# Optimization experiments

Measured on AMD Instinct MI355X. Metric: run time of the kernel, lower is better.

The kernel has to match this reference:

```python
import jax, jax.numpy as jnp
import numpy as np

E = 64          # num_routed_experts
K = 6           # num_experts_per_token
NS = 2          # num_shared_experts
D = 512         # hidden_size
F = 512         # expert_intermediate_size = intermediate_size // 4


def setup_inputs() -> dict:
    key = jax.random.key(0)
    ks = jax.random.split(key, 8)
    s = 0.02
    return {
        "hidden_states": jax.random.normal(ks[0], (2, 1024, D), dtype=jnp.float32),
        "Wr": jax.random.normal(ks[1], (D, E), dtype=jnp.float32) * s,      # router
        "sWg": jax.random.normal(ks[2], (NS, D, F), dtype=jnp.float32) * s,  # shared gate_proj
        "sWu": jax.random.normal(ks[3], (NS, D, F), dtype=jnp.float32) * s,  # shared up_proj
        "sWd": jax.random.normal(ks[4], (NS, F, D), dtype=jnp.float32) * s,  # shared down_proj
        "Wg": jax.random.normal(ks[5], (E, D, F), dtype=jnp.float32) * s,    # routed gate_proj
        "Wu": jax.random.normal(ks[6], (E, D, F), dtype=jnp.float32) * s,    # routed up_proj
        "Wd": jax.random.normal(ks[7], (E, F, D), dtype=jnp.float32) * s,    # routed down_proj
    }


def _swiglu_ffn(x, wg, wu, wd):
    # x: (N, D); wg/wu: (D, F); wd: (F, D)
    return (jax.nn.silu(x @ wg) * (x @ wu)) @ wd


def reference(hidden_states, Wr, sWg, sWu, sWd, Wg, Wu, Wd):
    B, S, d = hidden_states.shape
    x = hidden_states.reshape(-1, d)  # (N, D)
    N = x.shape[0]

    # ---- shared experts (always on) ----
    shared = jnp.zeros_like(x)
    for e in range(NS):
        shared = shared + _swiglu_ffn(x, sWg[e], sWu[e], sWd[e])

    # ---- top-k router ----
    logits = x @ Wr                                   # (N, E)
    probs = jax.nn.softmax(logits, axis=-1)
    top_w, top_i = jax.lax.top_k(probs, K)            # (N, K)
    top_w = top_w / jnp.sum(top_w, axis=-1, keepdims=True)  # renormalize
    gate = jnp.zeros((N, E), dtype=x.dtype).at[jnp.arange(N)[:, None], top_i].set(top_w)

    # ---- routed experts: per-expert FFN, combined with sparse gate ----
    routed = jnp.zeros_like(x)
    for e in range(E):
        routed = routed + _swiglu_ffn(x, Wg[e], Wu[e], Wd[e]) * gate[:, e:e + 1]

    out = (shared + routed + x).reshape(B, S, d)
    return out
```

## Files before the change

kernel.cpp:

```cpp
#include <hip/hip_runtime.h>

#define N_TOK 2048
#define DD 512
#define FF 512
#define EE 64
#define TK 6
#define NG 66
#define RSLOT 12288
#define NSLOT 16384
#define BM 64
#define BN 64
#define BK 64
#define NKT 8
#define MAXT 320
#define MATSZ 262144

typedef float f32x4 __attribute__((ext_vector_type(4)));
typedef __bf16 bf16x8 __attribute__((ext_vector_type(8)));

__device__ __forceinline__ unsigned cvtpk(float lo, float hi) {
  unsigned r;
  asm("v_cvt_pk_bf16_f32 %0, %1, %2" : "=v"(r) : "v"(lo), "v"(hi));
  return r;
}

__device__ __forceinline__ void gll16(const void* g, void* l) {
  __builtin_amdgcn_global_load_lds(
      (const __attribute__((address_space(1))) unsigned int*)g,
      (__attribute__((address_space(3))) unsigned int*)l, 16, 0, 0);
}

__global__ __launch_bounds__(256) void convw_k(
    const float* __restrict__ Wg, const float* __restrict__ Wu, const float* __restrict__ Wd,
    const float* __restrict__ sWg, const float* __restrict__ sWu, const float* __restrict__ sWd,
    short* __restrict__ Wt) {
  int y = blockIdx.y;
  int kind = y / 66, idx = y % 66;
  const float* src;
  if (kind == 0)      src = (idx < EE) ? Wg + (size_t)idx * MATSZ : sWg + (size_t)(idx - EE) * MATSZ;
  else if (kind == 1) src = (idx < EE) ? Wu + (size_t)idx * MATSZ : sWu + (size_t)(idx - EE) * MATSZ;
  else                src = (idx < EE) ? Wd + (size_t)idx * MATSZ : sWd + (size_t)(idx - EE) * MATSZ;
  short* dst = Wt + (size_t)y * MATSZ;
  int f0 = blockIdx.x * 64;
  int lane = threadIdx.x & 63, w = threadIdx.x >> 6;
  int fl = lane & 15, dg = lane >> 4;
  const float* sp = src + (size_t)(dg * 8) * 512 + f0 + fl * 4;
  short* dp = dst + (size_t)(f0 + fl * 4) * 512 + dg * 8;
#pragma unroll 1
  for (int it = 0; it < 4; ++it) {
    int db = (it * 4 + w) * 32;
    f32x4 v[8];
#pragma unroll
    for (int jd = 0; jd < 8; ++jd)
      v[jd] = *(const f32x4*)(sp + (size_t)(db + jd) * 512);
#pragma unroll
    for (int jf = 0; jf < 4; ++jf) {
      uint4 o;
      o.x = cvtpk(v[0][jf], v[1][jf]);
      o.y = cvtpk(v[2][jf], v[3][jf]);
      o.z = cvtpk(v[4][jf], v[5][jf]);
      o.w = cvtpk(v[6][jf], v[7][jf]);
      *(uint4*)(dp + (size_t)jf * 512 + db) = o;
    }
  }
}

__global__ void convx_k(const float* __restrict__ x, short* __restrict__ Xb) {
  int i = blockIdx.x * 256 + threadIdx.x;
  const f32x4* p = (const f32x4*)(x + (size_t)i * 8);
  f32x4 v0 = p[0], v1 = p[1];
  uint4 o;
  o.x = cvtpk(v0[0], v0[1]); o.y = cvtpk(v0[2], v0[3]);
  o.z = cvtpk(v1[0], v1[1]); o.w = cvtpk(v1[2], v1[3]);
  *(uint4*)&Xb[(size_t)i * 8] = o;
}

__global__ __launch_bounds__(256) void router_k(
    const float* __restrict__ x, const float* __restrict__ Wr,
    int* __restrict__ top_i, float* __restrict__ top_w, int* __restrict__ cnt) {
  __shared__ float xs[16 * 512];
  __shared__ float part[4][16][64];
  int tid = threadIdx.x, lane = tid & 63, w = tid >> 6;
  int t0 = blockIdx.x * 16;
  const f32x4* xin = (const f32x4*)(x + (size_t)t0 * DD);
  f32x4* xs4 = (f32x4*)xs;
#pragma unroll
  for (int i = 0; i < 8; ++i) xs4[i * 256 + tid] = xin[i * 256 + tid];
  __syncthreads();
  float acc[16];
#pragma unroll
  for (int t = 0; t < 16; ++t) acc[t] = 0.f;
  for (int kk = 0; kk < 32; ++kk) {
    int k = w * 128 + kk * 4;
    float w0 = Wr[(size_t)(k + 0) * EE + lane];
    float w1 = Wr[(size_t)(k + 1) * EE + lane];
    float w2 = Wr[(size_t)(k + 2) * EE + lane];
    float w3 = Wr[(size_t)(k + 3) * EE + lane];
#pragma unroll
    for (int t = 0; t < 16; ++t) {
      f32x4 xv = *(const f32x4*)&xs[t * 512 + k];
      acc[t] = fmaf(xv[0], w0, acc[t]);
      acc[t] = fmaf(xv[1], w1, acc[t]);
      acc[t] = fmaf(xv[2], w2, acc[t]);
      acc[t] = fmaf(xv[3], w3, acc[t]);
    }
  }
#pragma unroll
  for (int t = 0; t < 16; ++t) part[w][t][lane] = acc[t];
  __syncthreads();
#pragma unroll
  for (int tt = 0; tt < 4; ++tt) {
    int t = w * 4 + tt;
    float l0 = part[0][t][lane] + part[1][t][lane] + part[2][t][lane] + part[3][t][lane];
    float m = l0;
#pragma unroll
    for (int s = 32; s; s >>= 1) m = fmaxf(m, __shfl_xor(m, s));
    float p = __expf(l0 - m);
    int wi[TK]; float wv[TK];
#pragma unroll
    for (int it = 0; it < TK; ++it) {
      float v = p;
#pragma unroll
      for (int s = 32; s; s >>= 1) v = fmaxf(v, __shfl_xor(v, s));
      unsigned long long b = __ballot(p == v);
      int idx = __ffsll((unsigned long long)b) - 1;
      wi[it] = idx; wv[it] = v;
      if (lane == idx) p = -1.f;
    }
    float wsum = 0.f;
#pragma unroll
    for (int it = 0; it < TK; ++it) wsum += wv[it];
    int tg = t0 + t;
    if (lane < TK) {
      int si = 0; float sv = 0.f;
#pragma unroll
      for (int it = 0; it < TK; ++it) if (lane == it) { si = wi[it]; sv = wv[it]; }
      top_i[tg * TK + lane] = si;
      top_w[tg * TK + lane] = sv / wsum;
      atomicAdd(&cnt[si], 1);
    }
  }
}

__global__ void offsets_k(const int* __restrict__ cnt, int* __restrict__ goff,
                          int* __restrict__ fill, int* __restrict__ wk_g,
                          int* __restrict__ wk_mt, int* __restrict__ nitems) {
  int i = threadIdx.x;
  fill[i] = 0;
  int c = cnt[i];
  int s = c;
#pragma unroll
  for (int d = 1; d < 64; d <<= 1) { int t = __shfl_up(s, d); if (i >= d) s += t; }
  goff[i] = s - c;
  if (i == 63) {
    goff[EE] = RSLOT;
    goff[EE + 1] = RSLOT + N_TOK;
    goff[EE + 2] = RSLOT + 2 * N_TOK;
  }
  int nt = (c + BM - 1) >> 6;
  int ts = nt;
#pragma unroll
  for (int d = 1; d < 64; d <<= 1) { int t = __shfl_up(ts, d); if (i >= d) ts += t; }
  int texcl = ts - nt;
  for (int t = 0; t < nt; ++t) { wk_g[texcl + t] = i; wk_mt[texcl + t] = t; }
  int tot = __shfl(ts, 63);
  wk_g[tot + i] = EE + (i >> 5);
  wk_mt[tot + i] = i & 31;
  if (i == 0) nitems[0] = tot + 64;
}

__global__ void scatter_k(const int* __restrict__ top_i, const float* __restrict__ top_w,
                          const int* __restrict__ goff, int* __restrict__ fill,
                          int* __restrict__ btok, float* __restrict__ bw) {
  int idx = blockIdx.x * blockDim.x + threadIdx.x;
  if (idx < RSLOT) {
    int e = top_i[idx];
    int pos = goff[e] + atomicAdd(&fill[e], 1);
    btok[pos] = idx / TK;
    bw[pos] = top_w[idx];
  } else if (idx < NSLOT) {
    int j = idx - RSLOT;
    btok[idx] = j & (N_TOK - 1);
    bw[idx] = 1.0f;
  }
}

__global__ void initout_k(const float* __restrict__ x, float* __restrict__ out, int n4) {
  int i = blockIdx.x * blockDim.x + threadIdx.x;
  if (i < n4) reinterpret_cast<f32x4*>(out)[i] = reinterpret_cast<const f32x4*>(x)[i];
}

__global__ __launch_bounds__(256) void gemm1_k(
    const short* __restrict__ Xb, const short* __restrict__ Wtg, const short* __restrict__ Wtu,
    const int* __restrict__ goff, const int* __restrict__ btok,
    const int* __restrict__ wk_g, const int* __restrict__ wk_mt,
    const int* __restrict__ nitems, short* __restrict__ H) {
  int item = blockIdx.y;
  if (item >= nitems[0]) return;
  int g = wk_g[item], mt = wk_mt[item];
  int s0g = goff[g], cnt = goff[g + 1] - s0g;
  int n0 = blockIdx.x * BN;
  const short* gmat = Wtg + (size_t)g * MATSZ;
  const short* umat = Wtu + (size_t)g * MATSZ;

  __shared__ __align__(16) short lds[2][12288];

  int tid = threadIdx.x, lane = tid & 63, w = tid >> 6;
  int wr = w >> 1, wc = w & 1;
  int lr = lane & 15, lgq = lane >> 4;
  int s0 = s0g + mt * BM;

  const short* sp[6];
  int ldst[6];
#pragma unroll
  for (int q = 0; q < 6; ++q) {
    int c = w * 6 + q;
    ldst[q] = c * 512;
    int rl = (c & 7) * 8 + (lane >> 3);
    int u = (lane & 7) ^ (rl & 7);
    if (c < 8) {
      int slot = (mt * BM + rl < cnt) ? s0 + rl : s0;
      sp[q] = Xb + (size_t)btok[slot] * 512 + u * 8;
    } else if (c < 16) {
      sp[q] = gmat + (size_t)(n0 + rl) * 512 + u * 8;
    } else {
      sp[q] = umat + (size_t)(n0 + rl) * 512 + u * 8;
    }
  }

  f32x4 accg[2][2], accu[2][2];
#pragma unroll
  for (int i = 0; i < 2; ++i)
#pragma unroll
    for (int j = 0; j < 2; ++j) {
      accg[i][j] = f32x4{0.f, 0.f, 0.f, 0.f};
      accu[i][j] = f32x4{0.f, 0.f, 0.f, 0.f};
    }

  auto STAGE = [&](int b, int kt) {
#pragma unroll
    for (int q = 0; q < 6; ++q) gll16(sp[q] + kt * 64, &lds[b][ldst[q]]);
  };
  auto COMPUTE = [&](int b) {
    const short* L = lds[b];
#pragma unroll
    for (int ks = 0; ks < 2; ++ks) {
      bf16x8 af[2], bg[2], bu[2];
#pragma unroll
      for (int i = 0; i < 2; ++i) {
        int row = wr * 32 + i * 16 + lr;
        af[i] = *(const bf16x8*)&L[row * 64 + (((ks * 4 + lgq) ^ (row & 7)) * 8)];
      }
#pragma unroll
      for (int j = 0; j < 2; ++j) {
        int fr = wc * 32 + j * 16 + lr;
        int o = fr * 64 + (((ks * 4 + lgq) ^ (fr & 7)) * 8);
        bg[j] = *(const bf16x8*)&L[4096 + o];
        bu[j] = *(const bf16x8*)&L[8192 + o];
      }
#pragma unroll
      for (int i = 0; i < 2; ++i)
#pragma unroll
        for (int j = 0; j < 2; ++j) {
          accg[i][j] = __builtin_amdgcn_mfma_f32_16x16x32_bf16(af[i], bg[j], accg[i][j], 0, 0, 0);
          accu[i][j] = __builtin_amdgcn_mfma_f32_16x16x32_bf16(af[i], bu[j], accu[i][j], 0, 0, 0);
        }
    }
  };

  STAGE(0, 0);
  __syncthreads();
  int b = 0;
#pragma unroll 1
  for (int kt = 0; kt < NKT; ++kt) {
    if (kt + 1 < NKT) STAGE(b ^ 1, kt + 1);
    COMPUTE(b);
    __syncthreads();
    b ^= 1;
  }

#pragma unroll
  for (int i = 0; i < 2; ++i)
#pragma unroll
    for (int j = 0; j < 2; ++j)
#pragma unroll
      for (int r = 0; r < 4; ++r) {
        int mrow = wr * 32 + i * 16 + lgq * 4 + r;
        if (mt * BM + mrow < cnt) {
          float gg = accg[i][j][r];
          float uu = accu[i][j][r];
          float hv = (gg / (1.f + __expf(-gg))) * uu;
          int col = n0 + wc * 32 + j * 16 + lr;
          H[(size_t)(s0 + mrow) * FF + col] = (short)(cvtpk(hv, hv) & 0xffffu);
        }
      }
}

__global__ __launch_bounds__(256) void gemm2_k(
    const short* __restrict__ H, const short* __restrict__ Wtd,
    const int* __restrict__ goff, const int* __restrict__ btok, const float* __restrict__ bw,
    const int* __restrict__ wk_g, const int* __restrict__ wk_mt,
    const int* __restrict__ nitems, float* __restrict__ out) {
  int item = blockIdx.y;
  if (item >= nitems[0]) return;
  int g = wk_g[item], mt = wk_mt[item];
  int s0g = goff[g], cnt = goff[g + 1] - s0g;
  int n0 = blockIdx.x * BN;
  const short* dmat = Wtd + (size_t)g * MATSZ;

  __shared__ __align__(16) short lds[2][8192];

  int tid = threadIdx.x, lane = tid & 63, w = tid >> 6;
  int wr = w >> 1, wc = w & 1;
  int lr = lane & 15, lgq = lane >> 4;
  int s0 = s0g + mt * BM;

  const short* sp[4];
  int ldst[4];
#pragma unroll
  for (int q = 0; q < 4; ++q) {
    int c = w * 4 + q;
    ldst[q] = c * 512;
    int rl = (c & 7) * 8 + (lane >> 3);
    int u = (lane & 7) ^ (rl & 7);
    if (c < 8) {
      int slot = (mt * BM + rl < cnt) ? s0 + rl : s0;
      sp[q] = H + (size_t)slot * 512 + u * 8;
    } else {
      sp[q] = dmat + (size_t)(n0 + rl) * 512 + u * 8;
    }
  }

  f32x4 acc[2][2];
#pragma unroll
  for (int i = 0; i < 2; ++i)
#pragma unroll
    for (int j = 0; j < 2; ++j) acc[i][j] = f32x4{0.f, 0.f, 0.f, 0.f};

  auto STAGE = [&](int b, int kt) {
#pragma unroll
    for (int q = 0; q < 4; ++q) gll16(sp[q] + kt * 64, &lds[b][ldst[q]]);
  };
  auto COMPUTE = [&](int b) {
    const short* L = lds[b];
#pragma unroll
    for (int ks = 0; ks < 2; ++ks) {
      bf16x8 af[2], bd[2];
#pragma unroll
      for (int i = 0; i < 2; ++i) {
        int row = wr * 32 + i * 16 + lr;
        af[i] = *(const bf16x8*)&L[row * 64 + (((ks * 4 + lgq) ^ (row & 7)) * 8)];
      }
#pragma unroll
      for (int j = 0; j < 2; ++j) {
        int dr = wc * 32 + j * 16 + lr;
        bd[j] = *(const bf16x8*)&L[4096 + dr * 64 + (((ks * 4 + lgq) ^ (dr & 7)) * 8)];
      }
#pragma unroll
      for (int i = 0; i < 2; ++i)
#pragma unroll
        for (int j = 0; j < 2; ++j)
          acc[i][j] = __builtin_amdgcn_mfma_f32_16x16x32_bf16(af[i], bd[j], acc[i][j], 0, 0, 0);
    }
  };

  STAGE(0, 0);
  __syncthreads();
  int b = 0;
#pragma unroll 1
  for (int kt = 0; kt < NKT; ++kt) {
    if (kt + 1 < NKT) STAGE(b ^ 1, kt + 1);
    COMPUTE(b);
    __syncthreads();
    b ^= 1;
  }

#pragma unroll
  for (int i = 0; i < 2; ++i)
#pragma unroll
    for (int r = 0; r < 4; ++r) {
      int mrow = wr * 32 + i * 16 + lgq * 4 + r;
      if (mt * BM + mrow < cnt) {
        int slot = s0 + mrow;
        int tok = btok[slot];
        float wv = bw[slot];
#pragma unroll
        for (int j = 0; j < 2; ++j) {
          int col = n0 + wc * 32 + j * 16 + lr;
          atomicAdd(&out[(size_t)tok * DD + col], acc[i][j][r] * wv);
        }
      }
    }
}

extern "C" void kernel_launch(void* const* d_in, const int* in_sizes, int n_in,
                              void* d_out, int out_size, void* d_ws, size_t ws_size,
                              hipStream_t stream) {
  const float* x   = (const float*)d_in[0];
  const float* Wr  = (const float*)d_in[1];
  const float* sWg = (const float*)d_in[2];
  const float* sWu = (const float*)d_in[3];
  const float* sWd = (const float*)d_in[4];
  const float* Wg  = (const float*)d_in[5];
  const float* Wu  = (const float*)d_in[6];
  const float* Wd  = (const float*)d_in[7];
  float* out = (float*)d_out;

  char* wsb = (char*)d_ws;
  size_t off = 0;
  short* Wt = (short*)(wsb + off);    off += (size_t)198 * MATSZ * 2;
  short* H  = (short*)(wsb + off);    off += (size_t)NSLOT * FF * 2;
  short* Xb = (short*)(wsb + off);    off += (size_t)N_TOK * DD * 2;
  int*   top_i = (int*)(wsb + off);   off += (size_t)RSLOT * 4;
  float* top_w = (float*)(wsb + off); off += (size_t)RSLOT * 4;
  int*   btok = (int*)(wsb + off);    off += (size_t)NSLOT * 4;
  float* bwt  = (float*)(wsb + off);  off += (size_t)NSLOT * 4;
  int*   cnt  = (int*)(wsb + off);    off += 256;
  int*   fill = (int*)(wsb + off);    off += 256;
  int*   goff = (int*)(wsb + off);    off += 512;
  int*   wk_g = (int*)(wsb + off);    off += MAXT * 4;
  int*   wk_mt = (int*)(wsb + off);   off += MAXT * 4;
  int*   nitems = (int*)(wsb + off);  off += 256;

  const short* Wtg = Wt;
  const short* Wtu = Wt + (size_t)66 * MATSZ;
  const short* Wtd = Wt + (size_t)132 * MATSZ;

  hipMemsetAsync(cnt, 0, 256, stream);
  convw_k<<<dim3(8, 198), 256, 0, stream>>>(Wg, Wu, Wd, sWg, sWu, sWd, Wt);
  convx_k<<<512, 256, 0, stream>>>(x, Xb);
  router_k<<<N_TOK / 16, 256, 0, stream>>>(x, Wr, top_i, top_w, cnt);
  offsets_k<<<1, 64, 0, stream>>>(cnt, goff, fill, wk_g, wk_mt, nitems);
  scatter_k<<<NSLOT / 256, 256, 0, stream>>>(top_i, top_w, goff, fill, btok, bwt);
  int n4 = out_size / 4;
  initout_k<<<(n4 + 255) / 256, 256, 0, stream>>>(x, out, n4);
  dim3 grid1(FF / BN, MAXT, 1);
  gemm1_k<<<grid1, 256, 0, stream>>>(Xb, Wtg, Wtu, goff, btok, wk_g, wk_mt, nitems, H);
  dim3 grid2(DD / BN, MAXT, 1);
  gemm2_k<<<grid2, 256, 0, stream>>>(H, Wtd, goff, btok, bwt, wk_g, wk_mt, nitems, out);
}
```

Before: 239.6 us.

## Replace atomic scatter-add in down-proj with per-slot bf16 outputs and a combine kernel

gemm2 no longer atomically adds fp32 results into the output. It writes each slot's weighted row as bf16 into a new slot buffer, and a new combine kernel gathers each token's 8 slot rows, sums them with the residual, and writes the output once. This removes the global atomic contention and the separate init-output kernel, at the cost of an extra 16 MB round trip and a bf16 rounding of partial results. Separately, the weight-conversion kernel now issues all 32 loads before converting, to raise memory-level parallelism at the cost of more registers.

New measurement: 224.8 us. -6.2%, faster.

```diff
diff --git a/kernel.cpp b/kernel.cpp
--- a/kernel.cpp
+++ b/kernel.cpp
@@ -46,20 +46,24 @@
   int fl = lane & 15, dg = lane >> 4;
   const float* sp = src + (size_t)(dg * 8) * 512 + f0 + fl * 4;
   short* dp = dst + (size_t)(f0 + fl * 4) * 512 + dg * 8;
-#pragma unroll 1
+  f32x4 v[4][8];
+#pragma unroll
   for (int it = 0; it < 4; ++it) {
     int db = (it * 4 + w) * 32;
-    f32x4 v[8];
 #pragma unroll
     for (int jd = 0; jd < 8; ++jd)
-      v[jd] = *(const f32x4*)(sp + (size_t)(db + jd) * 512);
+      v[it][jd] = *(const f32x4*)(sp + (size_t)(db + jd) * 512);
+  }
+#pragma unroll
+  for (int it = 0; it < 4; ++it) {
+    int db = (it * 4 + w) * 32;
 #pragma unroll
     for (int jf = 0; jf < 4; ++jf) {
       uint4 o;
-      o.x = cvtpk(v[0][jf], v[1][jf]);
-      o.y = cvtpk(v[2][jf], v[3][jf]);
-      o.z = cvtpk(v[4][jf], v[5][jf]);
-      o.w = cvtpk(v[6][jf], v[7][jf]);
+      o.x = cvtpk(v[it][0][jf], v[it][1][jf]);
+      o.y = cvtpk(v[it][2][jf], v[it][3][jf]);
+      o.z = cvtpk(v[it][4][jf], v[it][5][jf]);
+      o.w = cvtpk(v[it][6][jf], v[it][7][jf]);
       *(uint4*)(dp + (size_t)jf * 512 + db) = o;
     }
   }
@@ -171,23 +175,20 @@
 
 __global__ void scatter_k(const int* __restrict__ top_i, const float* __restrict__ top_w,
                           const int* __restrict__ goff, int* __restrict__ fill,
-                          int* __restrict__ btok, float* __restrict__ bw) {
+                          int* __restrict__ btok, float* __restrict__ bw,
+                          int* __restrict__ tslot) {
   int idx = blockIdx.x * blockDim.x + threadIdx.x;
   if (idx < RSLOT) {
     int e = top_i[idx];
     int pos = goff[e] + atomicAdd(&fill[e], 1);
     btok[pos] = idx / TK;
     bw[pos] = top_w[idx];
+    tslot[idx] = pos;
   } else if (idx < NSLOT) {
     int j = idx - RSLOT;
     btok[idx] = j & (N_TOK - 1);
     bw[idx] = 1.0f;
   }
-}
-
-__global__ void initout_k(const float* __restrict__ x, float* __restrict__ out, int n4) {
-  int i = blockIdx.x * blockDim.x + threadIdx.x;
-  if (i < n4) reinterpret_cast<f32x4*>(out)[i] = reinterpret_cast<const f32x4*>(x)[i];
 }
 
 __global__ __launch_bounds__(256) void gemm1_k(
@@ -298,9 +299,9 @@
 
 __global__ __launch_bounds__(256) void gemm2_k(
     const short* __restrict__ H, const short* __restrict__ Wtd,
-    const int* __restrict__ goff, const int* __restrict__ btok, const float* __restrict__ bw,
+    const int* __restrict__ goff, const float* __restrict__ bw,
     const int* __restrict__ wk_g, const int* __restrict__ wk_mt,
-    const int* __restrict__ nitems, float* __restrict__ out) {
+    const int* __restrict__ nitems, short* __restrict__ Osl) {
   int item = blockIdx.y;
   if (item >= nitems[0]) return;
   int g = wk_g[item], mt = wk_mt[item];
@@ -382,15 +383,45 @@
       int mrow = wr * 32 + i * 16 + lgq * 4 + r;
       if (mt * BM + mrow < cnt) {
         int slot = s0 + mrow;
-        int tok = btok[slot];
         float wv = bw[slot];
 #pragma unroll
         for (int j = 0; j < 2; ++j) {
           int col = n0 + wc * 32 + j * 16 + lr;
-          atomicAdd(&out[(size_t)tok * DD + col], acc[i][j][r] * wv);
+          Osl[(size_t)slot * DD + col] = (short)(cvtpk(acc[i][j][r] * wv, 0.f) & 0xffffu);
         }
       }
     }
+}
+
+__global__ __launch_bounds__(256) void combine_k(
+    const short* __restrict__ Osl, const float* __restrict__ x,
+    const int* __restrict__ tslot, float* __restrict__ out) {
+  int wv = threadIdx.x >> 6, lane = threadIdx.x & 63;
+  int t = blockIdx.x * 4 + wv;
+  int d0 = lane * 8;
+  const float* xp = x + (size_t)t * DD + d0;
+  f32x4 sa = *(const f32x4*)xp;
+  f32x4 sb = *(const f32x4*)(xp + 4);
+  int slots[8];
+#pragma unroll
+  for (int k = 0; k < 6; ++k) slots[k] = tslot[t * TK + k];
+  slots[6] = RSLOT + t;
+  slots[7] = RSLOT + N_TOK + t;
+#pragma unroll
+  for (int k = 0; k < 8; ++k) {
+    uint4 hv = *(const uint4*)&Osl[(size_t)slots[k] * DD + d0];
+    unsigned u[4] = {hv.x, hv.y, hv.z, hv.w};
+#pragma unroll
+    for (int q = 0; q < 4; ++q) {
+      float lo = __builtin_bit_cast(float, u[q] << 16);
+      float hi = __builtin_bit_cast(float, u[q] & 0xffff0000u);
+      if (q < 2) { sa[q * 2] += lo; sa[q * 2 + 1] += hi; }
+      else { sb[(q - 2) * 2] += lo; sb[(q - 2) * 2 + 1] += hi; }
+    }
+  }
+  float* op = out + (size_t)t * DD + d0;
+  *(f32x4*)op = sa;
+  *(f32x4*)(op + 4) = sb;
 }
 
 extern "C" void kernel_launch(void* const* d_in, const int* in_sizes, int n_in,
@@ -410,11 +441,13 @@
   size_t off = 0;
   short* Wt = (short*)(wsb + off);    off += (size_t)198 * MATSZ * 2;
   short* H  = (short*)(wsb + off);    off += (size_t)NSLOT * FF * 2;
+  short* Osl = (short*)(wsb + off);   off += (size_t)NSLOT * DD * 2;
   short* Xb = (short*)(wsb + off);    off += (size_t)N_TOK * DD * 2;
   int*   top_i = (int*)(wsb + off);   off += (size_t)RSLOT * 4;
   float* top_w = (float*)(wsb + off); off += (size_t)RSLOT * 4;
   int*   btok = (int*)(wsb + off);    off += (size_t)NSLOT * 4;
   float* bwt  = (float*)(wsb + off);  off += (size_t)NSLOT * 4;
+  int*   tslot = (int*)(wsb + off);   off += (size_t)RSLOT * 4;
   int*   cnt  = (int*)(wsb + off);    off += 256;
   int*   fill = (int*)(wsb + off);    off += 256;
   int*   goff = (int*)(wsb + off);    off += 512;
@@ -431,11 +464,10 @@
   convx_k<<<512, 256, 0, stream>>>(x, Xb);
   router_k<<<N_TOK / 16, 256, 0, stream>>>(x, Wr, top_i, top_w, cnt);
   offsets_k<<<1, 64, 0, stream>>>(cnt, goff, fill, wk_g, wk_mt, nitems);
-  scatter_k<<<NSLOT / 256, 256, 0, stream>>>(top_i, top_w, goff, fill, btok, bwt);
-  int n4 = out_size / 4;
-  initout_k<<<(n4 + 255) / 256, 256, 0, stream>>>(x, out, n4);
+  scatter_k<<<NSLOT / 256, 256, 0, stream>>>(top_i, top_w, goff, fill, btok, bwt, tslot);
   dim3 grid1(FF / BN, MAXT, 1);
   gemm1_k<<<grid1, 256, 0, stream>>>(Xb, Wtg, Wtu, goff, btok, wk_g, wk_mt, nitems, H);
   dim3 grid2(DD / BN, MAXT, 1);
-  gemm2_k<<<grid2, 256, 0, stream>>>(H, Wtd, goff, btok, bwt, wk_g, wk_mt, nitems, out);
-}
+  gemm2_k<<<grid2, 256, 0, stream>>>(H, Wtd, goff, bwt, wk_g, wk_mt, nitems, Osl);
+  combine_k<<<N_TOK / 4, 256, 0, stream>>>(Osl, x, tslot, out);
+}
```
